# Performance work log

Hardware: AMD Instinct MI355X
Metric: run time of the kernel (lower is better)

## Reference

```python
import jax, jax.numpy as jnp
from jax import lax
import numpy as np

DN = ('NCHW', 'OIHW', 'NCHW')
EPS = 1e-8
LRELU_SLOPE = 0.2
SQRT2 = np.float32(np.sqrt(2.0))


def _blur2d(x):
    # 5x5 binomial FIR, depthwise, padding=2, stride=1 (Blur2d(kernel_size=5, padding=2))
    k1 = jnp.array([1.0, 4.0, 6.0, 4.0, 1.0], dtype=x.dtype)
    k2 = jnp.outer(k1, k1)
    k2 = k2 / k2.sum()
    C = x.shape[1]
    kern = jnp.broadcast_to(k2, (C, 1, 5, 5))
    return lax.conv_general_dilated(x, kern, window_strides=(1, 1),
                                    padding=[(2, 2), (2, 2)],
                                    feature_group_count=C,
                                    dimension_numbers=DN)


def _second_moment_norm(x, g):
    # normalize by per-channel spatial second moment, learnable gain g [C]
    ms = jnp.mean(jnp.square(x), axis=(2, 3), keepdims=True)  # [B,C,1,1]
    return x * lax.rsqrt(ms + EPS) * g[None, :, None, None]


def _modulated_conv(x, w, b, style_w, style_b, s, stride, padding):
    # StyleGAN2 modulated conv with demodulation, grouped-conv batch trick
    B, I, H, W = x.shape
    O, _, kh, kw = w.shape
    scale = np.float32(1.0 / np.sqrt(I * kh * kw))
    style = s @ style_w.T + style_b[None, :]                      # [B, I]
    wm = scale * w[None] * style[:, None, :, None, None]          # [B,O,I,kh,kw]
    d = lax.rsqrt(jnp.sum(jnp.square(wm), axis=(2, 3, 4)) + EPS)  # [B,O]
    wm = wm * d[:, :, None, None, None]
    xg = x.reshape(1, B * I, H, W)
    wg = wm.reshape(B * O, I, kh, kw)
    out = lax.conv_general_dilated(xg, wg, window_strides=(stride, stride),
                                   padding=[(padding, padding), (padding, padding)],
                                   feature_group_count=B,
                                   dimension_numbers=DN)
    out = out.reshape(B, O, out.shape[2], out.shape[3])
    return out + b[None, :, None, None]


def setup_inputs() -> dict:
    key = jax.random.key(0)
    ks = jax.random.split(key, 5)
    B, I, O, S, H, W, K = 8, 256, 256, 512, 128, 128, 3
    x = jax.random.normal(ks[0], (B, I, H, W), dtype=jnp.float32)
    s = jax.random.normal(ks[1], (B, S), dtype=jnp.float32)
    conv_w = jax.random.normal(ks[2], (O, I, K, K), dtype=jnp.float32)
    conv_b = jnp.zeros((O,), dtype=jnp.float32)
    style_w = jax.random.normal(ks[3], (I, S), dtype=jnp.float32) / np.float32(np.sqrt(S))
    style_b = jnp.ones((I,), dtype=jnp.float32)  # StyleGAN2 init: bias=1
    norm_g = jnp.ones((I,), dtype=jnp.float32)
    return {"x": x, "s": s, "conv_w": conv_w, "conv_b": conv_b,
            "style_w": style_w, "style_b": style_b, "norm_g": norm_g}


def reference(x, s, conv_w, conv_b, style_w, style_b, norm_g):
    x = _blur2d(x)                                   # blur (stride != 1 path)
    x = _second_moment_norm(x, norm_g)               # second-moment norm
    x = _modulated_conv(x, conv_w, conv_b, style_w, style_b, s, stride=2, padding=1)
    x = jnp.where(x >= 0, x, LRELU_SLOPE * x) * SQRT2  # scaled LeakyReLU
    return x
```

## Files before the change

kernel.cpp:

```cpp
#include <hip/hip_runtime.h>
#include <hip/hip_bf16.h>
#include <math.h>

#define B 8
#define IC 256
#define OC 256
#define SDIM 512
#define H 128
#define W 128
#define OH 64
#define OW 64
#define EPS 1e-8f
#define SQRT2 1.41421356237309504880f
#define SCALE 0.02083333395421505f

#define RS 16640
#define PLANE 1081600

typedef unsigned short u16;
typedef unsigned int u32;
typedef __attribute__((ext_vector_type(8))) short s16x8;
typedef __attribute__((ext_vector_type(4))) float f32x4;

__global__ void wsq_kernel(const float* __restrict__ w, float* __restrict__ wsq) {
    int i = blockIdx.x * 256 + threadIdx.x;
    const float* p = w + (size_t)i * 9;
    float sum = 0.f;
    for (int k = 0; k < 9; ++k) sum = fmaf(p[k], p[k], sum);
    wsq[i] = sum;
}

__global__ __launch_bounds__(256) void style_demod_kernel(const float* __restrict__ s,
                                                          const float* __restrict__ sw,
                                                          const float* __restrict__ sb,
                                                          const float* __restrict__ wsq,
                                                          float* __restrict__ style,
                                                          float* __restrict__ demod,
                                                          float* __restrict__ ssq) {
    __shared__ float st[256];
    const int b = blockIdx.x;
    const int tid = threadIdx.x;
    const float4* sv = (const float4*)(s + (size_t)b * SDIM);
    const float4* wv = (const float4*)(sw + (size_t)tid * SDIM);
    float sum = 0.f;
    #pragma unroll 4
    for (int k = 0; k < 128; ++k) {
        float4 a4 = sv[k], b4 = wv[k];
        sum = fmaf(a4.x, b4.x, fmaf(a4.y, b4.y, fmaf(a4.z, b4.z, fmaf(a4.w, b4.w, sum))));
    }
    float styv = sum + sb[tid];
    style[(b << 8) + tid] = styv;
    st[tid] = styv;
    ssq[(b << 8) + tid] = 0.f;
    __syncthreads();
    const float4* wq = (const float4*)(wsq + (size_t)tid * 256);
    float acc = 0.f;
    #pragma unroll 4
    for (int k = 0; k < 64; ++k) {
        float4 q = wq[k];
        float s0 = st[4 * k], s1 = st[4 * k + 1], s2 = st[4 * k + 2], s3 = st[4 * k + 3];
        acc = fmaf(s0 * s0, q.x, fmaf(s1 * s1, q.y, fmaf(s2 * s2, q.z, fmaf(s3 * s3, q.w, acc))));
    }
    demod[(b << 8) + tid] = rsqrtf(SCALE * SCALE * acc + EPS);
}

__global__ __launch_bounds__(256, 6) void blurpack_kernel(const float* __restrict__ x,
                                                          __hip_bfloat16* __restrict__ xbp,
                                                          float* __restrict__ ssq) {
    __shared__ __align__(16) char smem[24576];
    u16 (*raw)[12][128]  = reinterpret_cast<u16(*)[12][128]>(smem);
    u16 (*pbuf)[2][2][544] = reinterpret_cast<u16(*)[2][2][544]>(smem);
    const int t = threadIdx.x;
    const int strip = blockIdx.x;
    const int ic0 = blockIdx.y << 3;
    const int b = blockIdx.z;

    #pragma unroll
    for (int k = 0; k < 6; ++k) {
        int sidx = t + (k << 8);
        int r = sidx >> 7;
        int ch = (sidx >> 4) & 7;
        int cg = sidx & 15;
        int gr = (strip << 3) - 2 + r;
        uint4 q = {0u, 0u, 0u, 0u};
        if (gr >= 0 && gr < H) {
            const float* p = x + (((size_t)(b * 256 + ic0 + ch)) << 14) + (gr << 7) + (cg << 3);
            float4 v0 = *(const float4*)p;
            float4 v1 = *(const float4*)(p + 4);
            u16* qp = (u16*)&q;
            const float* vv0 = &v0.x;
            const float* vv1 = &v1.x;
            #pragma unroll
            for (int j = 0; j < 4; ++j) {
                __hip_bfloat16 b0 = __float2bfloat16(vv0[j]);
                __hip_bfloat16 b1 = __float2bfloat16(vv1[j]);
                qp[j] = *(u16*)&b0;
                qp[4 + j] = *(u16*)&b1;
            }
        }
        *(uint4*)&raw[ch][r][cg << 3] = q;
    }
    __syncthreads();

    const int hr = t >> 7;
    const int ch = (t >> 4) & 7;
    const int cg = t & 15;
    float ssacc = 0.f;
    uint2 res0[4], res1[4];

    #pragma unroll
    for (int pass = 0; pass < 4; ++pass) {
        const int br = (pass << 1) + hr;

        float v[8];
        {
            uint4 q0 = *(const uint4*)&raw[ch][br + 0][cg << 3];
            uint4 q1 = *(const uint4*)&raw[ch][br + 1][cg << 3];
            uint4 q2 = *(const uint4*)&raw[ch][br + 2][cg << 3];
            uint4 q3 = *(const uint4*)&raw[ch][br + 3][cg << 3];
            uint4 q4 = *(const uint4*)&raw[ch][br + 4][cg << 3];
            const u16* h0 = (const u16*)&q0; const u16* h1 = (const u16*)&q1;
            const u16* h2 = (const u16*)&q2; const u16* h3 = (const u16*)&q3;
            const u16* h4 = (const u16*)&q4;
            #pragma unroll
            for (int j = 0; j < 8; ++j) {
                float f0 = __uint_as_float(((u32)h0[j]) << 16);
                float f1 = __uint_as_float(((u32)h1[j]) << 16);
                float f2 = __uint_as_float(((u32)h2[j]) << 16);
                float f3 = __uint_as_float(((u32)h3[j]) << 16);
                float f4 = __uint_as_float(((u32)h4[j]) << 16);
                v[j] = fmaf(6.f, f2, fmaf(4.f, f1 + f3, f0 + f4));
            }
        }

        float vm2 = __shfl_up(v[6], 1, 64);
        float vm1 = __shfl_up(v[7], 1, 64);
        float vp1 = __shfl_down(v[0], 1, 64);
        float vp2 = __shfl_down(v[1], 1, 64);
        if (cg == 0)  { vm2 = 0.f; vm1 = 0.f; }
        if (cg == 15) { vp1 = 0.f; vp2 = 0.f; }
        float e[12];
        e[0] = vm2; e[1] = vm1;
        #pragma unroll
        for (int j = 0; j < 8; ++j) e[2 + j] = v[j];
        e[10] = vp1; e[11] = vp2;

        u16 hp[8];
        #pragma unroll
        for (int j = 0; j < 8; ++j) {
            float hv = fmaf(6.f, e[j + 2], fmaf(4.f, e[j + 1] + e[j + 3], e[j] + e[j + 4]))
                     * (1.0f / 256.0f);
            ssacc = fmaf(hv, hv, ssacc);
            __hip_bfloat16 hb = __float2bfloat16(hv);
            hp[j] = *(u16*)&hb;
        }
        u16 w0[4] = {hp[0], hp[2], hp[4], hp[6]};
        u16 w1[4] = {hp[1], hp[3], hp[5], hp[7]};
        res0[pass] = *(const uint2*)w0;
        res1[pass] = *(const uint2*)w1;
    }

    __syncthreads();

    #pragma unroll
    for (int pass = 0; pass < 4; ++pass) {
        *(uint2*)&pbuf[pass][hr][0][(ch << 6) + (cg << 2)] = res0[pass];
        *(uint2*)&pbuf[pass][hr][1][(ch << 6) + (cg << 2)] = res1[pass];
    }
    __syncthreads();

    {
        int fc = t & 127;
        int hr2 = t >> 7;
        int pw = fc & 1, pcol = fc >> 1;
        #pragma unroll
        for (int pass = 0; pass < 4; ++pass) {
            uint4 g;
            u16* gp = (u16*)&g;
            #pragma unroll
            for (int c2 = 0; c2 < 8; ++c2)
                gp[c2] = pbuf[pass][hr2][pw][(c2 << 6) + pcol];
            size_t off = (size_t)((b << 2) + (hr2 << 1) + pw) * PLANE
                       + (size_t)((strip << 2) + pass + 1) * RS
                       + (size_t)(pcol + 1) * 256 + ic0;
            *(uint4*)(xbp + off) = g;
        }
    }

    float sv2 = ssacc;
    sv2 += __shfl_down(sv2, 8, 16);
    sv2 += __shfl_down(sv2, 4, 16);
    sv2 += __shfl_down(sv2, 2, 16);
    sv2 += __shfl_down(sv2, 1, 16);
    if (cg == 0) atomicAdd(&ssq[(b << 8) + ic0 + ch], sv2);
}

__global__ void wf_kernel(const float* __restrict__ w,
                          const float* __restrict__ demod,
                          const float* __restrict__ ssq,
                          const float* __restrict__ style,
                          const float* __restrict__ g,
                          __hip_bfloat16* __restrict__ wf,
                          __hip_bfloat16* __restrict__ xbp) {
    int bo = blockIdx.x;
    int b = bo >> 8, o = bo & 255;
    int ic = threadIdx.x;
    float fac = rsqrtf(ssq[(b << 8) + ic] * (1.0f / 16384.0f) + EPS)
              * g[ic] * style[(b << 8) + ic] * SCALE;
    float m = demod[bo] * fac;
    const float* wp = w + ((size_t)o * 256 + ic) * 9;
    __hip_bfloat16* dst = wf + (size_t)bo * 2304 + ic;
    #pragma unroll
    for (int t = 0; t < 9; ++t)
        dst[t * 256] = __float2bfloat16(wp[t] * m);

    if (bo < 32) {
        int t = threadIdx.x;
        char* base = (char*)(xbp + (size_t)bo * PLANE);
        uint4 z = {0u, 0u, 0u, 0u};
        for (int k = 0; k < 9; ++k) {
            int c = t + (k << 8);
            if (c < 2080) *(uint4*)(base + (size_t)c * 16) = z;
        }
        for (int k = 0; k < 8; ++k) {
            int c = t + (k << 8);
            int r = 1 + (c >> 5);
            int off = (c & 31) << 3;
            *(uint4*)(base + ((size_t)r * RS + off) * 2) = z;
        }
    }
}

__device__ __forceinline__ void gl_lds16(const void* g, void* l) {
    __builtin_amdgcn_global_load_lds((const __attribute__((address_space(1))) u32*)g,
                                     (__attribute__((address_space(3))) u32*)l, 16, 0, 0);
}

__global__ __launch_bounds__(256, 2) void conv_kernel(const __hip_bfloat16* __restrict__ xbp,
                                                      const __hip_bfloat16* __restrict__ wf,
                                                      const float* __restrict__ bias,
                                                      float* __restrict__ out) {
    __shared__ char lds[65536];
    const int t = threadIdx.x;
    const int o0 = blockIdx.x << 7;
    const int y  = blockIdx.y;
    const int b  = blockIdx.z;
    const size_t bb = (size_t)b << 8;

    u32 aoffs[8], boffs[8];
    #pragma unroll
    for (int j = 0; j < 8; ++j) {
        int s = t + (j << 8);
        int r = s >> 4, m = s & 15;
        int g = m ^ (r & 7);
        aoffs[j] = (u32)(r * 2304 + (g << 3)) * 2;
        boffs[j] = (u32)((((y << 1) + (r >> 6)) * RS) + ((r & 63) << 8) + (g << 3)) * 2;
    }
    char* ldsA = lds;
    char* ldsB = lds + 32768;
    char* dstA = ldsA + t * 16;
    char* dstB = ldsB + t * 16;
    const char* gAbase = (const char*)(wf + (bb + o0) * 2304);

    const int lane = t & 63, wave = t >> 6;
    const int lr = lane & 15, quad = lane >> 4;
    const int mb = (wave & 1) << 6;
    const int nb = (wave >> 1) << 6;

    f32x4 acc[4][4];
    #pragma unroll
    for (int i = 0; i < 4; ++i)
        #pragma unroll
        for (int j = 0; j < 4; ++j) acc[i][j] = (f32x4){0.f, 0.f, 0.f, 0.f};

    for (int c = 0; c < 18; ++c) {
        int tap = c >> 1;
        int ich = (c & 1) << 7;
        int th = (tap * 11) >> 5;
        int tw = tap - th * 3;
        int ph  = (th == 1) ? 0 : 1;
        int dhp = (th == 0) ? 0 : 1;
        int pw  = (tw == 1) ? 0 : 1;
        int dwp = (tw == 0) ? 0 : 1;
        const char* gA = gAbase + (size_t)(tap * 256 + ich) * 2;
        const char* gB = (const char*)(xbp + (size_t)((b << 2) + (ph << 1) + pw) * PLANE
                                       + (size_t)dhp * RS + (dwp << 8) + ich);
        __syncthreads();
        #pragma unroll
        for (int j = 0; j < 8; ++j) gl_lds16(gA + aoffs[j], dstA + (j << 12));
        #pragma unroll
        for (int j = 0; j < 8; ++j) gl_lds16(gB + boffs[j], dstB + (j << 12));
        __syncthreads();

        #pragma unroll
        for (int s = 0; s < 4; ++s) {
            const int mq = ((s << 2) + quad) ^ (lr & 7);
            s16x8 a[4], bf[4];
            #pragma unroll
            for (int i = 0; i < 4; ++i)
                a[i] = *(const s16x8*)(ldsA + ((mb + (i << 4) + lr) << 8) + (mq << 4));
            #pragma unroll
            for (int j = 0; j < 4; ++j)
                bf[j] = *(const s16x8*)(ldsB + ((nb + (j << 4) + lr) << 8) + (mq << 4));
            #pragma unroll
            for (int i = 0; i < 4; ++i)
                #pragma unroll
                for (int j = 0; j < 4; ++j)
                    acc[i][j] = __builtin_amdgcn_mfma_f32_16x16x32_bf16(a[i], bf[j], acc[i][j], 0, 0, 0);
        }
    }

    float bi[4][4];
    #pragma unroll
    for (int i = 0; i < 4; ++i)
        #pragma unroll
        for (int rr = 0; rr < 4; ++rr)
            bi[i][rr] = bias[o0 + mb + (i << 4) + (quad << 2) + rr];
    const int n0 = y << 7;
    #pragma unroll
    for (int i = 0; i < 4; ++i) {
        #pragma unroll
        for (int j = 0; j < 4; ++j) {
            #pragma unroll
            for (int rr = 0; rr < 4; ++rr) {
                int oc = o0 + mb + (i << 4) + (quad << 2) + rr;
                int n = n0 + nb + (j << 4) + lr;
                int oh = n >> 6, ow2 = n & 63;
                float v = acc[i][j][rr] + bi[i][rr];
                v = (v >= 0.f ? v : 0.2f * v) * SQRT2;
                out[((bb + oc) << 12) + (oh << 6) + ow2] = v;
            }
        }
    }
}

extern "C" void kernel_launch(void* const* d_in, const int* in_sizes, int n_in,
                              void* d_out, int out_size, void* d_ws, size_t ws_size,
                              hipStream_t stream) {
    const float* x   = (const float*)d_in[0];
    const float* s   = (const float*)d_in[1];
    const float* cw  = (const float*)d_in[2];
    const float* cb  = (const float*)d_in[3];
    const float* sw  = (const float*)d_in[4];
    const float* sb  = (const float*)d_in[5];
    const float* ng  = (const float*)d_in[6];
    float* out = (float*)d_out;

    char* ws = (char*)d_ws;
    __hip_bfloat16* xbp = (__hip_bfloat16*)ws;
    __hip_bfloat16* wfb = (__hip_bfloat16*)(ws + 69222400);
    float* style  = (float*)(ws + 78659584);
    float* wsq    = style + 2048;
    float* demod  = wsq + 65536;
    float* ssq    = demod + 2048;

    wsq_kernel<<<256, 256, 0, stream>>>(cw, wsq);
    style_demod_kernel<<<8, 256, 0, stream>>>(s, sw, sb, wsq, style, demod, ssq);
    blurpack_kernel<<<dim3(16, 32, 8), 256, 0, stream>>>(x, xbp, ssq);
    wf_kernel<<<2048, 256, 0, stream>>>(cw, demod, ssq, style, ng, wfb, xbp);
    conv_kernel<<<dim3(2, 32, 8), 256, 0, stream>>>(xbp, wfb, cb, out);
}
```

Measured before the change: 323.2 us.

## Double-buffer conv LDS tiles with halved K-chunk to overlap loads and MFMA

The conv main loop now stages 64-channel K-chunks (36 iterations instead of 18 of 128 channels) into two alternating 32KB LDS buffers. The next chunk's global-to-LDS loads are issued before the MFMAs on the current chunk, so memory latency can hide behind compute, and there is one barrier per iteration instead of two. Row stride and swizzle are adapted to the 128-byte rows. The risks are more loop overhead per unit of work, and correctness now depends on the barrier waiting for the async LDS loads to finish.

```diff
diff --git a/kernel.cpp b/kernel.cpp
--- a/kernel.cpp
+++ b/kernel.cpp
@@ -247,19 +247,15 @@
     const int b  = blockIdx.z;
     const size_t bb = (size_t)b << 8;
 
-    u32 aoffs[8], boffs[8];
-    #pragma unroll
-    for (int j = 0; j < 8; ++j) {
+    u32 aoffs[4], boffs[4];
+    #pragma unroll
+    for (int j = 0; j < 4; ++j) {
         int s = t + (j << 8);
-        int r = s >> 4, m = s & 15;
+        int r = s >> 3, m = s & 7;
         int g = m ^ (r & 7);
         aoffs[j] = (u32)(r * 2304 + (g << 3)) * 2;
         boffs[j] = (u32)((((y << 1) + (r >> 6)) * RS) + ((r & 63) << 8) + (g << 3)) * 2;
     }
-    char* ldsA = lds;
-    char* ldsB = lds + 32768;
-    char* dstA = ldsA + t * 16;
-    char* dstB = ldsB + t * 16;
     const char* gAbase = (const char*)(wf + (bb + o0) * 2304);
 
     const int lane = t & 63, wave = t >> 6;
@@ -273,42 +269,56 @@
         #pragma unroll
         for (int j = 0; j < 4; ++j) acc[i][j] = (f32x4){0.f, 0.f, 0.f, 0.f};
 
-    for (int c = 0; c < 18; ++c) {
-        int tap = c >> 1;
-        int ich = (c & 1) << 7;
-        int th = (tap * 11) >> 5;
-        int tw = tap - th * 3;
-        int ph  = (th == 1) ? 0 : 1;
-        int dhp = (th == 0) ? 0 : 1;
-        int pw  = (tw == 1) ? 0 : 1;
-        int dwp = (tw == 0) ? 0 : 1;
-        const char* gA = gAbase + (size_t)(tap * 256 + ich) * 2;
-        const char* gB = (const char*)(xbp + (size_t)((b << 2) + (ph << 1) + pw) * PLANE
-                                       + (size_t)dhp * RS + (dwp << 8) + ich);
-        __syncthreads();
-        #pragma unroll
-        for (int j = 0; j < 8; ++j) gl_lds16(gA + aoffs[j], dstA + (j << 12));
-        #pragma unroll
-        for (int j = 0; j < 8; ++j) gl_lds16(gB + boffs[j], dstB + (j << 12));
-        __syncthreads();
-
-        #pragma unroll
-        for (int s = 0; s < 4; ++s) {
+    #define STAGE_TILE(cc, bufbase)                                                        \
+    {                                                                                      \
+        int tap = (cc) >> 2;                                                               \
+        int icq = ((cc) & 3) << 6;                                                         \
+        int th = (tap * 11) >> 5;                                                          \
+        int tw = tap - th * 3;                                                             \
+        int ph  = (th == 1) ? 0 : 1;                                                       \
+        int dhp = (th == 0) ? 0 : 1;                                                       \
+        int pw  = (tw == 1) ? 0 : 1;                                                       \
+        int dwp = (tw == 0) ? 0 : 1;                                                       \
+        const char* gA = gAbase + (size_t)(tap * 256 + icq) * 2;                           \
+        const char* gB = (const char*)(xbp + (size_t)((b << 2) + (ph << 1) + pw) * PLANE   \
+                                       + (size_t)dhp * RS + (dwp << 8) + icq);             \
+        char* dA = (bufbase) + t * 16;                                                     \
+        char* dB = (bufbase) + 16384 + t * 16;                                             \
+        _Pragma("unroll")                                                                  \
+        for (int j = 0; j < 4; ++j) gl_lds16(gA + aoffs[j], dA + (j << 12));               \
+        _Pragma("unroll")                                                                  \
+        for (int j = 0; j < 4; ++j) gl_lds16(gB + boffs[j], dB + (j << 12));               \
+    }
+
+    STAGE_TILE(0, lds);
+    __syncthreads();
+
+    int cur = 0;
+    for (int c = 0; c < 36; ++c) {
+        if (c < 35) STAGE_TILE(c + 1, lds + ((cur ^ 1) << 15));
+
+        const char* ldsA = lds + (cur << 15);
+        const char* ldsB = ldsA + 16384;
+        #pragma unroll
+        for (int s = 0; s < 2; ++s) {
             const int mq = ((s << 2) + quad) ^ (lr & 7);
             s16x8 a[4], bf[4];
             #pragma unroll
             for (int i = 0; i < 4; ++i)
-                a[i] = *(const s16x8*)(ldsA + ((mb + (i << 4) + lr) << 8) + (mq << 4));
+                a[i] = *(const s16x8*)(ldsA + ((mb + (i << 4) + lr) << 7) + (mq << 4));
             #pragma unroll
             for (int j = 0; j < 4; ++j)
-                bf[j] = *(const s16x8*)(ldsB + ((nb + (j << 4) + lr) << 8) + (mq << 4));
+                bf[j] = *(const s16x8*)(ldsB + ((nb + (j << 4) + lr) << 7) + (mq << 4));
             #pragma unroll
             for (int i = 0; i < 4; ++i)
                 #pragma unroll
                 for (int j = 0; j < 4; ++j)
                     acc[i][j] = __builtin_amdgcn_mfma_f32_16x16x32_bf16(a[i], bf[j], acc[i][j], 0, 0, 0);
         }
-    }
+        __syncthreads();
+        cur ^= 1;
+    }
+    #undef STAGE_TILE
 
     float bi[4][4];
     #pragma unroll
```

Result: no change. 317.5 us (-1.8%).
